# Performance work log

Hardware: AMD Instinct MI355X
Metric: run time of the kernel (lower is better)

The kernel has to match this reference:

```python
import jax, jax.numpy as jnp
import numpy as np

N_NODES = 50000
N_EDGES = 25000  # hyperedges
NNZ = 400000     # incidence pairs


def _segment_mean(x, idx, num_segments):
    s = jax.ops.segment_sum(x, idx, num_segments=num_segments)
    cnt = jax.ops.segment_sum(jnp.ones((x.shape[0], 1), x.dtype), idx, num_segments=num_segments)
    return s / jnp.maximum(cnt, 1.0)


def _unigcn_conv(X, W, vertex, edges, degE, degV):
    # X: [N, Cin] -> [N, Cout]
    X = X @ W                                   # linear (no bias)
    Xve = X[vertex]                             # gather per incidence [nnz, C]
    Xe = _segment_mean(Xve, edges, N_EDGES)     # first_aggregate='mean' over hyperedges
    Xe = Xe * degE                              # [M,1] scale
    Xev = Xe[edges]                             # gather back [nnz, C]
    Xv = jax.ops.segment_sum(Xev, vertex, num_segments=N_NODES)
    return Xv * degV                            # [N,1] scale


def setup_inputs() -> dict:
    key = jax.random.key(0)
    ks = jax.random.split(key, 8)
    nfeat, nhid_total, nclass = 512, 512, 40
    def glorot(k, fan_in, fan_out):
        std = np.sqrt(6.0 / (fan_in + fan_out))
        return jax.random.uniform(k, (fan_in, fan_out), jnp.float32, -std, std)
    return {
        "X": jax.random.normal(ks[0], (N_NODES, nfeat), jnp.float32),
        "vertex": jax.random.randint(ks[1], (NNZ,), 0, N_NODES, jnp.int32),
        "edges": jax.random.randint(ks[2], (NNZ,), 0, N_EDGES, jnp.int32),
        "W1": glorot(ks[3], nfeat, nhid_total),
        "W2": glorot(ks[4], nhid_total, nhid_total),
        "Wout": glorot(ks[5], nhid_total, nclass),
        "degE": jax.random.uniform(ks[6], (N_EDGES, 1), jnp.float32, 0.1, 1.0),
        "degV": jax.random.uniform(ks[7], (N_NODES, 1), jnp.float32, 0.1, 1.0),
    }


def reference(X, vertex, edges, W1, W2, Wout, degE, degV):
    # dropout layers are identity at eval (rates = 0)
    X = jax.nn.relu(_unigcn_conv(X, W1, vertex, edges, degE, degV))
    X = jax.nn.relu(_unigcn_conv(X, W2, vertex, edges, degE, degV))
    X = _unigcn_conv(X, Wout, vertex, edges, degE, degV)
    return jax.nn.log_softmax(X, axis=1)
```

## Files before the change

kernel.cpp:

```cpp
#include <hip/hip_runtime.h>

#define N_NODES 50000
#define N_EDGES_C 25000
#define NNZ_C 400000
#define SCHUNK 2048

typedef __bf16 bf16;
typedef __bf16 bf16x8 __attribute__((ext_vector_type(8)));
typedef __bf16 bf16x4 __attribute__((ext_vector_type(4)));
typedef float f32x4 __attribute__((ext_vector_type(4)));

typedef __attribute__((address_space(1))) const void as1_cvoid;
typedef __attribute__((address_space(3))) void as3_void;

__device__ __forceinline__ void gload_lds16(const bf16* g, bf16* l) {
  __builtin_amdgcn_global_load_lds((as1_cvoid*)g, (as3_void*)l, 16, 0, 0);
}

__global__ void hist_kernel(const int* __restrict__ vtx, const int* __restrict__ edg,
                            int* __restrict__ cntV, int* __restrict__ cntE, int nnz) {
  int i = blockIdx.x * blockDim.x + threadIdx.x;
  if (i < nnz) {
    atomicAdd(&cntV[vtx[i]], 1);
    atomicAdd(&cntE[edg[i]], 1);
  }
}

__global__ void scan_part(const int* __restrict__ cnt, int* __restrict__ part, int n) {
  __shared__ int red[256];
  const int b = blockIdx.x, t = threadIdx.x;
  const int base = b * SCHUNK + t * 8;
  int s = 0;
#pragma unroll
  for (int q = 0; q < 8; ++q) {
    int i = base + q;
    if (i < n) s += cnt[i];
  }
  red[t] = s;
  __syncthreads();
  for (int d = 128; d > 0; d >>= 1) {
    if (t < d) red[t] += red[t + d];
    __syncthreads();
  }
  if (t == 0) part[b] = red[0];
}

__global__ void scan_mid(int* __restrict__ part, int* __restrict__ off, int nparts, int n) {
  const int lane = threadIdx.x;
  int orig = (lane < nparts) ? part[lane] : 0;
  int v = orig;
  for (int o = 1; o < 64; o <<= 1) {
    int x = __shfl_up(v, o);
    if (lane >= o) v += x;
  }
  if (lane < nparts) part[lane] = v - orig;
  if (lane == 63) off[n] = v;
}

__global__ void scan_final(const int* __restrict__ cnt, const int* __restrict__ part,
                           int* __restrict__ off, int n) {
  __shared__ int tsum[256];
  const int b = blockIdx.x, t = threadIdx.x;
  const int base = b * SCHUNK + t * 8;
  int loc[8];
  int s = 0;
#pragma unroll
  for (int q = 0; q < 8; ++q) {
    int i = base + q;
    loc[q] = (i < n) ? cnt[i] : 0;
    s += loc[q];
  }
  tsum[t] = s;
  __syncthreads();
  for (int d = 1; d < 256; d <<= 1) {
    int x = (t >= d) ? tsum[t - d] : 0;
    __syncthreads();
    tsum[t] += x;
    __syncthreads();
  }
  int run = part[b] + ((t > 0) ? tsum[t - 1] : 0);
#pragma unroll
  for (int q = 0; q < 8; ++q) {
    int i = base + q;
    if (i < n) off[i] = run;
    run += loc[q];
  }
}

__global__ void scatter_kernel(const int* __restrict__ vtx, const int* __restrict__ edg,
                               const int* __restrict__ eoff, const int* __restrict__ voff,
                               int* __restrict__ curE, int* __restrict__ curV,
                               int* __restrict__ evtx, int* __restrict__ vedg, int nnz) {
  int i = blockIdx.x * blockDim.x + threadIdx.x;
  if (i < nnz) {
    int e = edg[i], v = vtx[i];
    int p = atomicAdd(&curE[e], 1);
    evtx[eoff[e] + p] = v;
    int q = atomicAdd(&curV[v], 1);
    vedg[voff[v] + q] = e;
  }
}

__global__ void convert_f2b(const float* __restrict__ in, bf16* __restrict__ out, size_t n) {
  size_t i = ((size_t)blockIdx.x * blockDim.x + threadIdx.x) * 4;
  if (i >= n) return;
  float4 v = *(const float4*)(in + i);
  bf16x4 o;
  o[0] = (bf16)v.x; o[1] = (bf16)v.y; o[2] = (bf16)v.z; o[3] = (bf16)v.w;
  *(bf16x4*)(out + i) = o;
}

__global__ void transpose_w(const float* __restrict__ W, bf16* __restrict__ Wt,
                            int K, int N, int NtRows) {
  int idx = blockIdx.x * blockDim.x + threadIdx.x;
  int total = NtRows * K;
  if (idx >= total) return;
  int n = idx / K;
  int k = idx - n * K;
  Wt[idx] = (n < N) ? (bf16)W[(size_t)k * N + n] : (bf16)0.0f;
}

template <int BF16OUT>
__global__ __launch_bounds__(256) void gemm_bf16_kernel(
    const bf16* __restrict__ A, const bf16* __restrict__ B,
    float* __restrict__ Cf, bf16* __restrict__ Cb, int M, int K, int ldC, int Nstore) {
  __shared__ bf16 Al[128][64];
  __shared__ bf16 Bl[128][64];
  const int t = threadIdx.x;
  const int m0 = blockIdx.x * 128;
  const int n0 = blockIdx.y * 128;
  const int w = t >> 6, lane = t & 63;
  const int wr = w >> 1, wc = w & 1;
  const int lr = lane & 15;
  const int ls = lane >> 4;

  f32x4 acc[4][4];
#pragma unroll
  for (int m = 0; m < 4; ++m)
#pragma unroll
    for (int n = 0; n < 4; ++n) acc[m][n] = (f32x4){0.f, 0.f, 0.f, 0.f};

  const int srow = lane >> 3;
  const int scol = ((lane & 7) ^ ((lane >> 3) & 7)) << 3;

  for (int kk = 0; kk < K; kk += 64) {
#pragma unroll
    for (int q = 0; q < 4; ++q) {
      const int row = w * 32 + q * 8 + srow;
      gload_lds16(A + (size_t)(m0 + row) * K + kk + scol, &Al[w * 32 + q * 8][0]);
      gload_lds16(B + (size_t)(n0 + row) * K + kk + scol, &Bl[w * 32 + q * 8][0]);
    }
    __syncthreads();
#pragma unroll
    for (int ks = 0; ks < 2; ++ks) {
      bf16x8 af[4], bfr[4];
#pragma unroll
      for (int m = 0; m < 4; ++m) {
        const int R = wr * 64 + m * 16 + lr;
        af[m] = *(const bf16x8*)(&Al[R][((ks * 4 + ls) ^ (lr & 7)) << 3]);
      }
#pragma unroll
      for (int n = 0; n < 4; ++n) {
        const int R = wc * 64 + n * 16 + lr;
        bfr[n] = *(const bf16x8*)(&Bl[R][((ks * 4 + ls) ^ (lr & 7)) << 3]);
      }
#pragma unroll
      for (int m = 0; m < 4; ++m)
#pragma unroll
        for (int n = 0; n < 4; ++n)
          acc[m][n] = __builtin_amdgcn_mfma_f32_16x16x32_bf16(af[m], bfr[n], acc[m][n], 0, 0, 0);
    }
    __syncthreads();
  }

  const int cr = (lane >> 4) << 2;
  const int cc = lane & 15;
#pragma unroll
  for (int m = 0; m < 4; ++m) {
#pragma unroll
    for (int n = 0; n < 4; ++n) {
      int gc = n0 + wc * 64 + n * 16 + cc;
      if (gc >= Nstore) continue;
#pragma unroll
      for (int i = 0; i < 4; ++i) {
        int gr = m0 + wr * 64 + m * 16 + cr + i;
        if (gr < M) {
          if (BF16OUT) Cb[(size_t)gr * ldC + gc] = (bf16)acc[m][n][i];
          else         Cf[(size_t)gr * ldC + gc] = acc[m][n][i];
        }
      }
    }
  }
}

__global__ __launch_bounds__(256) void edge_agg_w(
    const bf16* __restrict__ Y, const int* __restrict__ eoff, const int* __restrict__ evtx,
    const float* __restrict__ degE, bf16* __restrict__ Xe, int nE) {
  const int wv = (blockIdx.x * 256 + threadIdx.x) >> 6;
  if (wv >= nE) return;
  const int lane = threadIdx.x & 63;
  const int beg = eoff[wv], end = eoff[wv + 1];
  const int cnt = end - beg;
  const float scale = (cnt > 0) ? degE[wv] / (float)cnt : 0.f;
  float acc[8] = {0.f, 0.f, 0.f, 0.f, 0.f, 0.f, 0.f, 0.f};
  for (int base = beg; base < end; base += 64) {
    const int nb = min(64, end - base);
    int myidx = (lane < nb) ? evtx[base + lane] : 0;
    int j = 0;
    for (; j + 3 < nb; j += 4) {
      const int i0 = __shfl(myidx, j);
      const int i1 = __shfl(myidx, j + 1);
      const int i2 = __shfl(myidx, j + 2);
      const int i3 = __shfl(myidx, j + 3);
      bf16x8 v0 = *(const bf16x8*)(Y + (size_t)i0 * 512 + lane * 8);
      bf16x8 v1 = *(const bf16x8*)(Y + (size_t)i1 * 512 + lane * 8);
      bf16x8 v2 = *(const bf16x8*)(Y + (size_t)i2 * 512 + lane * 8);
      bf16x8 v3 = *(const bf16x8*)(Y + (size_t)i3 * 512 + lane * 8);
#pragma unroll
      for (int q = 0; q < 8; ++q)
        acc[q] += ((float)v0[q] + (float)v1[q]) + ((float)v2[q] + (float)v3[q]);
    }
    for (; j < nb; ++j) {
      const int i0 = __shfl(myidx, j);
      bf16x8 v0 = *(const bf16x8*)(Y + (size_t)i0 * 512 + lane * 8);
#pragma unroll
      for (int q = 0; q < 8; ++q) acc[q] += (float)v0[q];
    }
  }
  bf16x8 o;
#pragma unroll
  for (int q = 0; q < 8; ++q) o[q] = (bf16)(acc[q] * scale);
  *(bf16x8*)(Xe + (size_t)wv * 512 + lane * 8) = o;
}

__global__ __launch_bounds__(256) void vtx_agg_w(
    const bf16* __restrict__ Xe, const int* __restrict__ voff, const int* __restrict__ vedg,
    const float* __restrict__ degV, bf16* __restrict__ outB, int nV) {
  const int wv = (blockIdx.x * 256 + threadIdx.x) >> 6;
  if (wv >= nV) return;
  const int lane = threadIdx.x & 63;
  const int beg = voff[wv], end = voff[wv + 1];
  const float dv = degV[wv];
  float acc[8] = {0.f, 0.f, 0.f, 0.f, 0.f, 0.f, 0.f, 0.f};
  for (int base = beg; base < end; base += 64) {
    const int nb = min(64, end - base);
    int myidx = (lane < nb) ? vedg[base + lane] : 0;
    int j = 0;
    for (; j + 3 < nb; j += 4) {
      const int i0 = __shfl(myidx, j);
      const int i1 = __shfl(myidx, j + 1);
      const int i2 = __shfl(myidx, j + 2);
      const int i3 = __shfl(myidx, j + 3);
      bf16x8 v0 = *(const bf16x8*)(Xe + (size_t)i0 * 512 + lane * 8);
      bf16x8 v1 = *(const bf16x8*)(Xe + (size_t)i1 * 512 + lane * 8);
      bf16x8 v2 = *(const bf16x8*)(Xe + (size_t)i2 * 512 + lane * 8);
      bf16x8 v3 = *(const bf16x8*)(Xe + (size_t)i3 * 512 + lane * 8);
#pragma unroll
      for (int q = 0; q < 8; ++q)
        acc[q] += ((float)v0[q] + (float)v1[q]) + ((float)v2[q] + (float)v3[q]);
    }
    for (; j < nb; ++j) {
      const int i0 = __shfl(myidx, j);
      bf16x8 v0 = *(const bf16x8*)(Xe + (size_t)i0 * 512 + lane * 8);
#pragma unroll
      for (int q = 0; q < 8; ++q) acc[q] += (float)v0[q];
    }
  }
  bf16x8 o;
#pragma unroll
  for (int q = 0; q < 8; ++q) o[q] = (bf16)fmaxf(acc[q] * dv, 0.f);
  *(bf16x8*)(outB + (size_t)wv * 512 + lane * 8) = o;
}

__global__ __launch_bounds__(256) void edge_agg40_w(
    const float* __restrict__ Y, const int* __restrict__ eoff, const int* __restrict__ evtx,
    const float* __restrict__ degE, float* __restrict__ Xe, int nE) {
  const int wv = (blockIdx.x * 256 + threadIdx.x) >> 6;
  if (wv >= nE) return;
  const int lane = threadIdx.x & 63;
  const int beg = eoff[wv], end = eoff[wv + 1];
  const int cnt = end - beg;
  const float scale = (cnt > 0) ? degE[wv] / (float)cnt : 0.f;
  float a0 = 0.f;
  for (int base = beg; base < end; base += 64) {
    const int nb = min(64, end - base);
    int myidx = (lane < nb) ? evtx[base + lane] : 0;
    int j = 0;
    for (; j + 3 < nb; j += 4) {
      const int i0 = __shfl(myidx, j);
      const int i1 = __shfl(myidx, j + 1);
      const int i2 = __shfl(myidx, j + 2);
      const int i3 = __shfl(myidx, j + 3);
      if (lane < 40) {
        float x0 = Y[(size_t)i0 * 40 + lane];
        float x1 = Y[(size_t)i1 * 40 + lane];
        float x2 = Y[(size_t)i2 * 40 + lane];
        float x3 = Y[(size_t)i3 * 40 + lane];
        a0 += (x0 + x1) + (x2 + x3);
      }
    }
    for (; j < nb; ++j) {
      const int i0 = __shfl(myidx, j);
      if (lane < 40) a0 += Y[(size_t)i0 * 40 + lane];
    }
  }
  if (lane < 40) Xe[(size_t)wv * 40 + lane] = a0 * scale;
}

__global__ __launch_bounds__(256) void vtx_agg_lsm(
    const float* __restrict__ Xe, const int* __restrict__ voff, const int* __restrict__ vedg,
    const float* __restrict__ degV, float* __restrict__ out, int nV) {
  const int wv = (blockIdx.x * 256 + threadIdx.x) >> 6;
  if (wv >= nV) return;
  const int lane = threadIdx.x & 63;
  const int beg = voff[wv], end = voff[wv + 1];
  const float dv = degV[wv];
  float a0 = 0.f;
  for (int base = beg; base < end; base += 64) {
    const int nb = min(64, end - base);
    int myidx = (lane < nb) ? vedg[base + lane] : 0;
    int j = 0;
    for (; j + 3 < nb; j += 4) {
      const int i0 = __shfl(myidx, j);
      const int i1 = __shfl(myidx, j + 1);
      const int i2 = __shfl(myidx, j + 2);
      const int i3 = __shfl(myidx, j + 3);
      if (lane < 40) {
        float x0 = Xe[(size_t)i0 * 40 + lane];
        float x1 = Xe[(size_t)i1 * 40 + lane];
        float x2 = Xe[(size_t)i2 * 40 + lane];
        float x3 = Xe[(size_t)i3 * 40 + lane];
        a0 += (x0 + x1) + (x2 + x3);
      }
    }
    for (; j < nb; ++j) {
      const int i0 = __shfl(myidx, j);
      if (lane < 40) a0 += Xe[(size_t)i0 * 40 + lane];
    }
  }
  a0 *= dv;
  float val = (lane < 40) ? a0 : -3.4e38f;
  float m = val;
#pragma unroll
  for (int o = 32; o > 0; o >>= 1) m = fmaxf(m, __shfl_xor(m, o));
  float ex = (lane < 40) ? expf(val - m) : 0.f;
  float s = ex;
#pragma unroll
  for (int o = 32; o > 0; o >>= 1) s += __shfl_xor(s, o);
  float ls = logf(s);
  if (lane < 40) out[(size_t)wv * 40 + lane] = val - m - ls;
}

extern "C" void kernel_launch(void* const* d_in, const int* in_sizes, int n_in,
                              void* d_out, int out_size, void* d_ws, size_t ws_size,
                              hipStream_t stream) {
  (void)in_sizes; (void)n_in; (void)out_size; (void)ws_size;
  const float* X = (const float*)d_in[0];
  const int* vertex = (const int*)d_in[1];
  const int* edges = (const int*)d_in[2];
  const float* W1 = (const float*)d_in[3];
  const float* W2 = (const float*)d_in[4];
  const float* Wout = (const float*)d_in[5];
  const float* degE = (const float*)d_in[6];
  const float* degV = (const float*)d_in[7];
  float* out = (float*)d_out;

  char* ws = (char*)d_ws;
  size_t off = 0;
  auto alloc = [&](size_t bytes) -> void* {
    void* p = ws + off;
    off += (bytes + 255) & ~(size_t)255;
    return p;
  };
  bf16* Xb  = (bf16*)alloc((size_t)N_NODES * 512 * sizeof(bf16));
  bf16* Yb  = (bf16*)alloc((size_t)N_NODES * 512 * sizeof(bf16));
  bf16* XeB = (bf16*)alloc((size_t)N_EDGES_C * 512 * sizeof(bf16));
  float* Y40  = (float*)alloc((size_t)N_NODES * 40 * sizeof(float));
  float* Xe40 = (float*)alloc((size_t)N_EDGES_C * 40 * sizeof(float));
  bf16* Wt  = (bf16*)alloc((size_t)512 * 512 * sizeof(bf16));
  int* eoff = (int*)alloc((N_EDGES_C + 1) * sizeof(int));
  int* voff = (int*)alloc((N_NODES + 1) * sizeof(int));
  int* evtx = (int*)alloc((size_t)NNZ_C * sizeof(int));
  int* vedg = (int*)alloc((size_t)NNZ_C * sizeof(int));
  int* cntE = (int*)alloc(N_EDGES_C * sizeof(int));
  int* cntV = (int*)alloc(N_NODES * sizeof(int));
  int* curE = (int*)alloc(N_EDGES_C * sizeof(int));
  int* curV = (int*)alloc(N_NODES * sizeof(int));
  int* partE = (int*)alloc(64 * sizeof(int));
  int* partV = (int*)alloc(64 * sizeof(int));

  hipMemsetAsync(cntE, 0, N_EDGES_C * sizeof(int), stream);
  hipMemsetAsync(cntV, 0, N_NODES * sizeof(int), stream);
  hipMemsetAsync(curE, 0, N_EDGES_C * sizeof(int), stream);
  hipMemsetAsync(curV, 0, N_NODES * sizeof(int), stream);

  hist_kernel<<<(NNZ_C + 255) / 256, 256, 0, stream>>>(vertex, edges, cntV, cntE, NNZ_C);

  const int nbE = (N_EDGES_C + SCHUNK - 1) / SCHUNK;
  const int nbV = (N_NODES + SCHUNK - 1) / SCHUNK;
  scan_part<<<nbE, 256, 0, stream>>>(cntE, partE, N_EDGES_C);
  scan_mid<<<1, 64, 0, stream>>>(partE, eoff, nbE, N_EDGES_C);
  scan_final<<<nbE, 256, 0, stream>>>(cntE, partE, eoff, N_EDGES_C);
  scan_part<<<nbV, 256, 0, stream>>>(cntV, partV, N_NODES);
  scan_mid<<<1, 64, 0, stream>>>(partV, voff, nbV, N_NODES);
  scan_final<<<nbV, 256, 0, stream>>>(cntV, partV, voff, N_NODES);

  scatter_kernel<<<(NNZ_C + 255) / 256, 256, 0, stream>>>(vertex, edges, eoff, voff,
                                                          curE, curV, evtx, vedg, NNZ_C);

  convert_f2b<<<(N_NODES * 512 / 4 + 255) / 256, 256, 0, stream>>>(X, Xb, (size_t)N_NODES * 512);

  const int MB = (N_NODES + 127) / 128;

  transpose_w<<<(512 * 512 + 255) / 256, 256, 0, stream>>>(W1, Wt, 512, 512, 512);
  {
    dim3 g(MB, 4);
    gemm_bf16_kernel<1><<<g, 256, 0, stream>>>(Xb, Wt, nullptr, Yb, N_NODES, 512, 512, 512);
  }
  edge_agg_w<<<(N_EDGES_C + 3) / 4, 256, 0, stream>>>(Yb, eoff, evtx, degE, XeB, N_EDGES_C);
  vtx_agg_w<<<(N_NODES + 3) / 4, 256, 0, stream>>>(XeB, voff, vedg, degV, Xb, N_NODES);

  transpose_w<<<(512 * 512 + 255) / 256, 256, 0, stream>>>(W2, Wt, 512, 512, 512);
  {
    dim3 g(MB, 4);
    gemm_bf16_kernel<1><<<g, 256, 0, stream>>>(Xb, Wt, nullptr, Yb, N_NODES, 512, 512, 512);
  }
  edge_agg_w<<<(N_EDGES_C + 3) / 4, 256, 0, stream>>>(Yb, eoff, evtx, degE, XeB, N_EDGES_C);
  vtx_agg_w<<<(N_NODES + 3) / 4, 256, 0, stream>>>(XeB, voff, vedg, degV, Xb, N_NODES);

  transpose_w<<<(128 * 512 + 255) / 256, 256, 0, stream>>>(Wout, Wt, 512, 40, 128);
  {
    dim3 g(MB, 1);
    gemm_bf16_kernel<0><<<g, 256, 0, stream>>>(Xb, Wt, Y40, nullptr, N_NODES, 512, 40, 40);
  }
  edge_agg40_w<<<(N_EDGES_C + 3) / 4, 256, 0, stream>>>(Y40, eoff, evtx, degE, Xe40, N_EDGES_C);
  vtx_agg_lsm<<<(N_NODES + 3) / 4, 256, 0, stream>>>(Xe40, voff, vedg, degV, out, N_NODES);
}
```

Before: 542.6 us.

## Double-buffer GEMM LDS tiles and shrink gather unroll in aggregation kernels

```diff
diff --git a/kernel.cpp b/kernel.cpp
--- a/kernel.cpp
+++ b/kernel.cpp
@@ -124,8 +124,8 @@
 __global__ __launch_bounds__(256) void gemm_bf16_kernel(
     const bf16* __restrict__ A, const bf16* __restrict__ B,
     float* __restrict__ Cf, bf16* __restrict__ Cb, int M, int K, int ldC, int Nstore) {
-  __shared__ bf16 Al[128][64];
-  __shared__ bf16 Bl[128][64];
+  __shared__ bf16 Al[2][128][64];
+  __shared__ bf16 Bl[2][128][64];
   const int t = threadIdx.x;
   const int m0 = blockIdx.x * 128;
   const int n0 = blockIdx.y * 128;
@@ -140,29 +140,47 @@
 #pragma unroll
     for (int n = 0; n < 4; ++n) acc[m][n] = (f32x4){0.f, 0.f, 0.f, 0.f};
 
-  const int srow = lane >> 3;
-  const int scol = ((lane & 7) ^ ((lane >> 3) & 7)) << 3;
-
-  for (int kk = 0; kk < K; kk += 64) {
-#pragma unroll
-    for (int q = 0; q < 4; ++q) {
-      const int row = w * 32 + q * 8 + srow;
-      gload_lds16(A + (size_t)(m0 + row) * K + kk + scol, &Al[w * 32 + q * 8][0]);
-      gload_lds16(B + (size_t)(n0 + row) * K + kk + scol, &Bl[w * 32 + q * 8][0]);
-    }
-    __syncthreads();
+  const int srow8 = lane >> 3;
+  const int scol = ((lane & 7) ^ srow8) << 3;
+
+  const bf16* Abase = A + (size_t)m0 * K;
+  const bf16* Bbase = B + (size_t)n0 * K;
+
+#define STAGE(tile, bsel)                                                        \
+  {                                                                              \
+    const int kk_ = (tile) * 64;                                                 \
+    _Pragma("unroll")                                                            \
+    for (int q = 0; q < 4; ++q) {                                                \
+      const int row = w * 32 + q * 8 + srow8;                                    \
+      gload_lds16(Abase + (size_t)row * K + kk_ + scol, &Al[bsel][w*32+q*8][0]); \
+      gload_lds16(Bbase + (size_t)row * K + kk_ + scol, &Bl[bsel][w*32+q*8][0]); \
+    }                                                                            \
+  }
+
+  const int NT = K >> 6;
+  STAGE(0, 0);
+  for (int tt = 0; tt < NT; ++tt) {
+    const int cur = tt & 1;
+    if (tt + 1 < NT) {
+      STAGE(tt + 1, cur ^ 1);
+      asm volatile("s_waitcnt vmcnt(8)" ::: "memory");
+    } else {
+      asm volatile("s_waitcnt vmcnt(0)" ::: "memory");
+    }
+    __builtin_amdgcn_s_barrier();
+    __builtin_amdgcn_s_setprio(1);
 #pragma unroll
     for (int ks = 0; ks < 2; ++ks) {
       bf16x8 af[4], bfr[4];
 #pragma unroll
       for (int m = 0; m < 4; ++m) {
         const int R = wr * 64 + m * 16 + lr;
-        af[m] = *(const bf16x8*)(&Al[R][((ks * 4 + ls) ^ (lr & 7)) << 3]);
+        af[m] = *(const bf16x8*)(&Al[cur][R][((ks * 4 + ls) ^ (lr & 7)) << 3]);
       }
 #pragma unroll
       for (int n = 0; n < 4; ++n) {
         const int R = wc * 64 + n * 16 + lr;
-        bfr[n] = *(const bf16x8*)(&Bl[R][((ks * 4 + ls) ^ (lr & 7)) << 3]);
+        bfr[n] = *(const bf16x8*)(&Bl[cur][R][((ks * 4 + ls) ^ (lr & 7)) << 3]);
       }
 #pragma unroll
       for (int m = 0; m < 4; ++m)
@@ -170,8 +188,10 @@
         for (int n = 0; n < 4; ++n)
           acc[m][n] = __builtin_amdgcn_mfma_f32_16x16x32_bf16(af[m], bfr[n], acc[m][n], 0, 0, 0);
     }
-    __syncthreads();
-  }
+    __builtin_amdgcn_s_setprio(0);
+    __builtin_amdgcn_s_barrier();
+  }
+#undef STAGE
 
   const int cr = (lane >> 4) << 2;
   const int cc = lane & 15;
@@ -207,20 +227,15 @@
     const int nb = min(64, end - base);
     int myidx = (lane < nb) ? evtx[base + lane] : 0;
     int j = 0;
-    for (; j + 3 < nb; j += 4) {
+    for (; j + 1 < nb; j += 2) {
       const int i0 = __shfl(myidx, j);
       const int i1 = __shfl(myidx, j + 1);
-      const int i2 = __shfl(myidx, j + 2);
-      const int i3 = __shfl(myidx, j + 3);
       bf16x8 v0 = *(const bf16x8*)(Y + (size_t)i0 * 512 + lane * 8);
       bf16x8 v1 = *(const bf16x8*)(Y + (size_t)i1 * 512 + lane * 8);
-      bf16x8 v2 = *(const bf16x8*)(Y + (size_t)i2 * 512 + lane * 8);
-      bf16x8 v3 = *(const bf16x8*)(Y + (size_t)i3 * 512 + lane * 8);
-#pragma unroll
-      for (int q = 0; q < 8; ++q)
-        acc[q] += ((float)v0[q] + (float)v1[q]) + ((float)v2[q] + (float)v3[q]);
-    }
-    for (; j < nb; ++j) {
+#pragma unroll
+      for (int q = 0; q < 8; ++q) acc[q] += (float)v0[q] + (float)v1[q];
+    }
+    if (j < nb) {
       const int i0 = __shfl(myidx, j);
       bf16x8 v0 = *(const bf16x8*)(Y + (size_t)i0 * 512 + lane * 8);
 #pragma unroll
@@ -246,20 +261,15 @@
     const int nb = min(64, end - base);
     int myidx = (lane < nb) ? vedg[base + lane] : 0;
     int j = 0;
-    for (; j + 3 < nb; j += 4) {
+    for (; j + 1 < nb; j += 2) {
       const int i0 = __shfl(myidx, j);
       const int i1 = __shfl(myidx, j + 1);
-      const int i2 = __shfl(myidx, j + 2);
-      const int i3 = __shfl(myidx, j + 3);
       bf16x8 v0 = *(const bf16x8*)(Xe + (size_t)i0 * 512 + lane * 8);
       bf16x8 v1 = *(const bf16x8*)(Xe + (size_t)i1 * 512 + lane * 8);
-      bf16x8 v2 = *(const bf16x8*)(Xe + (size_t)i2 * 512 + lane * 8);
-      bf16x8 v3 = *(const bf16x8*)(Xe + (size_t)i3 * 512 + lane * 8);
-#pragma unroll
-      for (int q = 0; q < 8; ++q)
-        acc[q] += ((float)v0[q] + (float)v1[q]) + ((float)v2[q] + (float)v3[q]);
-    }
-    for (; j < nb; ++j) {
+#pragma unroll
+      for (int q = 0; q < 8; ++q) acc[q] += (float)v0[q] + (float)v1[q];
+    }
+    if (j < nb) {
       const int i0 = __shfl(myidx, j);
       bf16x8 v0 = *(const bf16x8*)(Xe + (size_t)i0 * 512 + lane * 8);
 #pragma unroll
```

After: 543.7 us. About the same (+0.2%).
